# Kernel optimization log

Measured on AMD Instinct MI355X. Metric: run time of the kernel, lower is better.

Reference implementation:

```python
import jax, jax.numpy as jnp
import numpy as np
from jax.scipy.special import logsumexp

EPS = 0.05        # entropic regularization (blur^p)
N_ITERS = 20      # Sinkhorn iterations
N, M, D = 8192, 8192, 64


def setup_inputs() -> dict:
    key = jax.random.key(0)
    k1, k2, k3, k4 = jax.random.split(key, 4)
    return {
        "a": jax.random.uniform(k1, (N,), dtype=jnp.float32),
        "x": jax.random.normal(k2, (N, D), dtype=jnp.float32),
        "b": jax.random.uniform(k3, (M,), dtype=jnp.float32),
        "y": jax.random.normal(k4, (M, D), dtype=jnp.float32),
    }


def reference(a, x, b, y):
    eps = EPS
    # _normalize_weights: probability simplex
    a = a / jnp.sum(a)
    b = b / jnp.sum(b)
    loga = jnp.log(a)
    logb = jnp.log(b)
    # squared-Euclidean cost C_ij = ||x_i - y_j||^2, built via one GEMM (online kernel's math)
    x2 = jnp.sum(x * x, axis=1)            # [N]
    y2 = jnp.sum(y * y, axis=1)            # [M]
    C = x2[:, None] + y2[None, :] - 2.0 * (x @ y.T)   # [N, M]

    # log-domain Sinkhorn: f_i = -eps * LSE_j( log b_j + (g_j - C_ij)/eps )
    def softmin_rows(g_, C_, logw):   # reduce over columns j -> [N]
        return -eps * logsumexp(logw[None, :] + (g_[None, :] - C_) / eps, axis=1)

    def softmin_cols(f_, C_, logw):   # reduce over rows i -> [M]
        return -eps * logsumexp(logw[:, None] + (f_[:, None] - C_) / eps, axis=0)

    def body(i, fg):
        f_, g_ = fg
        f_ = softmin_rows(g_, C, logb)
        g_ = softmin_cols(f_, C, loga)
        return (f_, g_)

    f0 = jnp.zeros_like(a)
    g0 = jnp.zeros_like(b)
    f, g = jax.lax.fori_loop(0, N_ITERS, body, (f0, g0))

    # GeomLoss-style: one final symmetric update from detached potentials (Danskin)
    f_d = jax.lax.stop_gradient(f)
    g_d = jax.lax.stop_gradient(g)
    f_fin = softmin_rows(g_d, C, logb)
    g_fin = softmin_cols(f_d, C, loga)
    # OT_eps(a, b) = <a, f> + <b, g>
    return jnp.sum(a * f_fin) + jnp.sum(b * g_fin)
```

## Files before the change

### kernel.cpp

```cpp
#include <hip/hip_runtime.h>
#include <hip/hip_bf16.h>

#define EPS       0.05f
#define N_ITERS   20
#define NR        8192
#define DIM       64
#define LOG2E     1.4426950408889634f
#define LN2       0.6931471805599453f
#define S2        (2.0f * LOG2E / EPS)
#define EPSLN2    (EPS * LN2)
#define NEGINF    (-1e30f)
#define NSPLIT    16

typedef __attribute__((ext_vector_type(8))) short short8;
typedef __attribute__((ext_vector_type(4))) float float4v;

#define GLD_LDS16(src, dst)                                              \
    __builtin_amdgcn_global_load_lds(                                    \
        (const __attribute__((address_space(1))) void*)(src),            \
        (__attribute__((address_space(3))) void*)(dst), 16, 0, 0)

__device__ __forceinline__ float wave_reduce_sum(float v) {
    #pragma unroll
    for (int m = 1; m < 64; m <<= 1) v += __shfl_xor(v, m, 64);
    return v;
}

__device__ __forceinline__ float merge16_l(const float2* __restrict__ P, int i) {
    float2 p[NSPLIT];
    float M = NEGINF;
    #pragma unroll
    for (int k = 0; k < NSPLIT; k++) {
        p[k] = P[k * NR + i];
        M = fmaxf(M, p[k].x);
    }
    float S = 0.f;
    #pragma unroll
    for (int k = 0; k < NSPLIT; k++)
        S += p[k].y * __builtin_amdgcn_exp2f(p[k].x - M);
    return M + __builtin_amdgcn_logf(S);
}

__global__ void sums_kernel(const float* __restrict__ a, const float* __restrict__ b,
                            float* __restrict__ sums) {
    __shared__ float red[32];
    int tid = threadIdx.x;
    float pa = 0.f, pb = 0.f;
    for (int i = tid; i < NR; i += blockDim.x) { pa += a[i]; pb += b[i]; }
    pa = wave_reduce_sum(pa);
    pb = wave_reduce_sum(pb);
    int wid = tid >> 6, ln = tid & 63;
    if (ln == 0) { red[wid] = pa; red[wid + 16] = pb; }
    __syncthreads();
    if (tid == 0) {
        float sa = 0.f, sb = 0.f;
        int nw = blockDim.x >> 6;
        for (int w = 0; w < nw; w++) { sa += red[w]; sb += red[w + 16]; }
        sums[0] = logf(sa); sums[1] = logf(sb); sums[2] = sa; sums[3] = sb;
    }
}

__global__ void prep_kernel(const float* __restrict__ x, const float* __restrict__ y,
                            const float* __restrict__ a, const float* __restrict__ b,
                            const float* __restrict__ sums,
                            short8* __restrict__ xs, short8* __restrict__ ys,
                            float* __restrict__ x2, float* __restrict__ y2,
                            float* __restrict__ la2, float* __restrict__ lb2,
                            float2* __restrict__ Pb) {
    int gid = blockIdx.x * 256 + threadIdx.x;
    bool isx = gid < NR * 8;
    int cid = isx ? gid : gid - NR * 8;
    int row = cid >> 3;
    int c   = cid & 7;
    const float4* src = (const float4*)(isx ? x : y);
    float4 v0 = src[row * 16 + c * 2];
    float4 v1 = src[row * 16 + c * 2 + 1];

    short8 st;
    st[0] = __bfloat16_as_short(__float2bfloat16(v0.x));
    st[1] = __bfloat16_as_short(__float2bfloat16(v0.y));
    st[2] = __bfloat16_as_short(__float2bfloat16(v0.z));
    st[3] = __bfloat16_as_short(__float2bfloat16(v0.w));
    st[4] = __bfloat16_as_short(__float2bfloat16(v1.x));
    st[5] = __bfloat16_as_short(__float2bfloat16(v1.y));
    st[6] = __bfloat16_as_short(__float2bfloat16(v1.z));
    st[7] = __bfloat16_as_short(__float2bfloat16(v1.w));

    int T = row >> 4, ln = row & 15, f = c >> 2, q = c & 3;
    (isx ? xs : ys)[T * 128 + f * 64 + q * 16 + ln] = st;

    float sq = v0.x*v0.x + v0.y*v0.y + v0.z*v0.z + v0.w*v0.w
             + v1.x*v1.x + v1.y*v1.y + v1.z*v1.z + v1.w*v1.w;
    #pragma unroll
    for (int m = 1; m < 8; m <<= 1) sq += __shfl_xor(sq, m, 64);

    if (c == 0) {
        if (isx) {
            x2[row] = sq;
            la2[row] = (logf(a[row]) - sums[0]) * LOG2E;
        } else {
            y2[row] = sq;
            lb2[row] = (logf(b[row]) - sums[1]) * LOG2E;
            Pb[row] = make_float2(sq * (LOG2E / EPS), 1.0f);
            #pragma unroll
            for (int k = 1; k < NSPLIT; k++)
                Pb[k * NR + row] = make_float2(NEGINF, 0.0f);
        }
    }
}

#define LSE4(acc, c4, mm, ss)                                            \
    {                                                                    \
        float z0 = fmaf(S2, (acc)[0], (c4).x);                           \
        float z1 = fmaf(S2, (acc)[1], (c4).y);                           \
        float z2 = fmaf(S2, (acc)[2], (c4).z);                           \
        float z3 = fmaf(S2, (acc)[3], (c4).w);                           \
        float zm = fmaxf(fmaxf(z0, z1), fmaxf(z2, z3));                  \
        float mn = fmaxf((mm), zm);                                      \
        float e  = __builtin_amdgcn_exp2f((mm) - mn);                    \
        float p  = (__builtin_amdgcn_exp2f(z0 - mn)                      \
                  + __builtin_amdgcn_exp2f(z1 - mn))                     \
                 + (__builtin_amdgcn_exp2f(z2 - mn)                      \
                  + __builtin_amdgcn_exp2f(z3 - mn));                    \
        (ss) = fmaf((ss), e, p);                                         \
        (mm) = mn;                                                       \
    }

__global__ __launch_bounds__(1024, 4) void pass_kernel(
        const short8* __restrict__ matXs,
        const short8* __restrict__ matYs,
        const float2* __restrict__ Pin,
        const float* __restrict__ lw2col,
        float2* __restrict__ Pout) {
    __shared__ __attribute__((aligned(16))) char xlds[65536];
    __shared__ __attribute__((aligned(16))) char ybuf[2][16384];
    __shared__ __attribute__((aligned(16))) float cbl[512];
    __shared__ float2 comb[512][5];

    const int tid = threadIdx.x;
    const int bi  = blockIdx.x;
    const int q   = bi & 15;
    const int rg  = bi >> 4;
    const int rb  = rg * 512;
    const int cb0 = q * 512;

    const int w    = tid >> 6;
    const int lane = tid & 63;
    const int quad = lane >> 4;
    const int ln   = lane & 15;
    const int cst  = w & 3;
    const int rq   = w >> 2;

    const char* xsrc = (const char*)matXs + (size_t)rb * 128;
    #pragma unroll
    for (int r = 0; r < 4; r++)
        GLD_LDS16(xsrc + r * 16384 + tid * 16, &xlds[r * 16384 + w * 1024]);
    const char* ysrc = (const char*)matYs + (size_t)cb0 * 128;
    GLD_LDS16(ysrc + 0 * 16384 + tid * 16, &ybuf[0][w * 1024]);
    GLD_LDS16(ysrc + 1 * 16384 + tid * 16, &ybuf[1][w * 1024]);
    __builtin_amdgcn_sched_barrier(0);

    if (tid < 512) {
        int j = cb0 + tid;
        cbl[tid] = lw2col[j] - merge16_l(Pin, j);
    }
    __builtin_amdgcn_sched_barrier(0);
    __builtin_amdgcn_s_waitcnt(0x0071);
    __builtin_amdgcn_s_barrier();
    __builtin_amdgcn_sched_barrier(0);

    short8 xf0[8], xf1[8];
    {
        const char* xw = &xlds[(rq * 8) * 2048];
        #pragma unroll
        for (int t = 0; t < 8; t++) {
            xf0[t] = *(const short8*)(xw + t * 2048 + lane * 16);
            xf1[t] = *(const short8*)(xw + t * 2048 + 1024 + lane * 16);
        }
    }

    float lm[8], ls[8];
    #pragma unroll
    for (int t = 0; t < 8; t++) { lm[t] = NEGINF; ls[t] = 0.f; }

    #pragma unroll
    for (int c = 0; c < 4; c++) {
        const char* base = &ybuf[c & 1][0];
        #pragma unroll
        for (int uu = 0; uu < 2; uu++) {
            const int u = cst * 2 + uu;
            short8 ya0 = *(const short8*)(base + u * 2048 + lane * 16);
            short8 ya1 = *(const short8*)(base + u * 2048 + 1024 + lane * 16);
            float4 c4  = *(const float4*)(cbl + (c * 8 + u) * 16 + quad * 4);

            #pragma unroll
            for (int tt = 0; tt < 8; tt++) {
                float4v acc = {0.f, 0.f, 0.f, 0.f};
                acc = __builtin_amdgcn_mfma_f32_16x16x32_bf16(ya0, xf0[tt], acc, 0, 0, 0);
                acc = __builtin_amdgcn_mfma_f32_16x16x32_bf16(ya1, xf1[tt], acc, 0, 0, 0);
                LSE4(acc, c4, lm[tt], ls[tt]);
            }
        }
        if (c < 3) {
            __builtin_amdgcn_sched_barrier(0);
            __builtin_amdgcn_s_barrier();
            __builtin_amdgcn_sched_barrier(0);
            if (c < 2)
                GLD_LDS16(ysrc + (c + 2) * 16384 + tid * 16, &ybuf[c & 1][w * 1024]);
            __builtin_amdgcn_sched_barrier(0);
            if (c < 2) __builtin_amdgcn_s_waitcnt(0x0071);
            else       __builtin_amdgcn_s_waitcnt(0x0070);
            __builtin_amdgcn_s_barrier();
            __builtin_amdgcn_sched_barrier(0);
        }
    }

    #pragma unroll
    for (int mask = 16; mask < 64; mask <<= 1) {
        #pragma unroll
        for (int t = 0; t < 8; t++) {
            float mo = __shfl_xor(lm[t], mask, 64);
            float so = __shfl_xor(ls[t], mask, 64);
            float M  = fmaxf(lm[t], mo);
            ls[t] = ls[t] * __builtin_amdgcn_exp2f(lm[t] - M)
                  + so    * __builtin_amdgcn_exp2f(mo    - M);
            lm[t] = M;
        }
    }

    __syncthreads();
    if (lane < 16) {
        #pragma unroll
        for (int t = 0; t < 8; t++)
            comb[rq * 128 + t * 16 + ln][cst] = make_float2(lm[t], ls[t]);
    }
    __syncthreads();

    if (tid < 512) {
        float2 cc0 = comb[tid][0];
        float M = cc0.x, S = cc0.y;
        #pragma unroll
        for (int cc = 1; cc < 4; cc++) {
            float2 p = comb[tid][cc];
            float Mn = fmaxf(M, p.x);
            S = S * __builtin_amdgcn_exp2f(M - Mn)
              + p.y * __builtin_amdgcn_exp2f(p.x - Mn);
            M = Mn;
        }
        Pout[q * NR + rb + tid] = make_float2(M, S);
    }
}

__global__ void reduce1_kernel(const float* __restrict__ a, const float* __restrict__ b,
                               const float* __restrict__ x2, const float* __restrict__ y2,
                               const float2* __restrict__ Pff, const float2* __restrict__ Pgf,
                               float2* __restrict__ red2) {
    __shared__ float red[4];
    int tid = threadIdx.x;
    int r   = blockIdx.x * 128 + (tid & 127);
    bool gs = tid >= 128;
    float L  = merge16_l(gs ? Pgf : Pff, r);
    float sq = gs ? y2[r] : x2[r];
    float wv = gs ? b[r]  : a[r];
    float v  = wv * (sq - EPSLN2 * L);
    v = wave_reduce_sum(v);
    if ((tid & 63) == 0) red[tid >> 6] = v;
    __syncthreads();
    if (tid == 0) red2[blockIdx.x] = make_float2(red[0] + red[1], red[2] + red[3]);
}

__global__ void reduce2_kernel(const float* __restrict__ sums,
                               const float2* __restrict__ red2,
                               float* __restrict__ out) {
    int tid = threadIdx.x;
    float2 v = red2[tid];
    float da = wave_reduce_sum(v.x);
    float db = wave_reduce_sum(v.y);
    if (tid == 0) out[0] = da / sums[2] + db / sums[3];
}

extern "C" void kernel_launch(void* const* d_in, const int* in_sizes, int n_in,
                              void* d_out, int out_size, void* d_ws, size_t ws_size,
                              hipStream_t stream) {
    const float* a = (const float*)d_in[0];
    const float* x = (const float*)d_in[1];
    const float* b = (const float*)d_in[2];
    const float* y = (const float*)d_in[3];

    char* ws = (char*)d_ws;
    short8* xs = (short8*)ws;
    short8* ys = (short8*)(ws + (1 << 20));
    float* fp  = (float*)(ws + (2 << 20));
    float* x2  = fp;
    float* y2  = fp + NR;
    float* la2 = fp + 2 * NR;
    float* lb2 = fp + 3 * NR;
    float2* P   = (float2*)(fp + 4 * NR);
    float2* Pf  = P;
    float2* Pb  = P + NSPLIT * NR;
    float2* Pff = P + 2 * NSPLIT * NR;
    float2* Pgf = P + 3 * NSPLIT * NR;
    float2* red2 = P + 4 * NSPLIT * NR;
    float* sums  = (float*)(red2 + 64);

    sums_kernel<<<1, 1024, 0, stream>>>(a, b, sums);
    prep_kernel<<<(2 * NR * 8) / 256, 256, 0, stream>>>(x, y, a, b, sums,
                                                        xs, ys,
                                                        x2, y2, la2, lb2, Pb);

    for (int it = 0; it < N_ITERS; it++) {
        pass_kernel<<<256, 1024, 0, stream>>>(xs, ys, Pb, lb2, Pf);
        pass_kernel<<<256, 1024, 0, stream>>>(ys, xs, Pf, la2, Pb);
    }
    pass_kernel<<<256, 1024, 0, stream>>>(xs, ys, Pb, lb2, Pff);
    pass_kernel<<<256, 1024, 0, stream>>>(ys, xs, Pf, la2, Pgf);

    reduce1_kernel<<<64, 256, 0, stream>>>(a, b, x2, y2, Pff, Pgf, red2);
    reduce2_kernel<<<1, 64, 0, stream>>>(sums, red2, (float*)d_out);
}
```

Before: 858.1 us.

## Fold cost scale into bf16 x and bias into MFMA accumulator; quad-buffer Y tiles

The S2 scale is folded into the bf16 x operand during prep, and the per-column bias is passed as the initial MFMA accumulator. This removes the per-element FMA in the logsumexp inner loop. The Y tile staging changes from a double buffer to four LDS buffers loaded up front, which drops the mid-loop reload and one barrier per chunk. The cost is 32KB more LDS per block, which may lower occupancy, and bf16 rounding now applies to the scaled x values.

```diff
diff --git a/kernel.cpp b/kernel.cpp
--- a/kernel.cpp
+++ b/kernel.cpp
@@ -76,15 +76,16 @@
     float4 v0 = src[row * 16 + c * 2];
     float4 v1 = src[row * 16 + c * 2 + 1];
 
+    const float sc = isx ? S2 : 1.0f;
     short8 st;
-    st[0] = __bfloat16_as_short(__float2bfloat16(v0.x));
-    st[1] = __bfloat16_as_short(__float2bfloat16(v0.y));
-    st[2] = __bfloat16_as_short(__float2bfloat16(v0.z));
-    st[3] = __bfloat16_as_short(__float2bfloat16(v0.w));
-    st[4] = __bfloat16_as_short(__float2bfloat16(v1.x));
-    st[5] = __bfloat16_as_short(__float2bfloat16(v1.y));
-    st[6] = __bfloat16_as_short(__float2bfloat16(v1.z));
-    st[7] = __bfloat16_as_short(__float2bfloat16(v1.w));
+    st[0] = __bfloat16_as_short(__float2bfloat16(v0.x * sc));
+    st[1] = __bfloat16_as_short(__float2bfloat16(v0.y * sc));
+    st[2] = __bfloat16_as_short(__float2bfloat16(v0.z * sc));
+    st[3] = __bfloat16_as_short(__float2bfloat16(v0.w * sc));
+    st[4] = __bfloat16_as_short(__float2bfloat16(v1.x * sc));
+    st[5] = __bfloat16_as_short(__float2bfloat16(v1.y * sc));
+    st[6] = __bfloat16_as_short(__float2bfloat16(v1.z * sc));
+    st[7] = __bfloat16_as_short(__float2bfloat16(v1.w * sc));
 
     int T = row >> 4, ln = row & 15, f = c >> 2, q = c & 3;
     (isx ? xs : ys)[T * 128 + f * 64 + q * 16 + ln] = st;
@@ -109,14 +110,11 @@
     }
 }
 
-#define LSE4(acc, c4, mm, ss)                                            \
+#define LSE4(acc, mm, ss)                                                \
     {                                                                    \
-        float z0 = fmaf(S2, (acc)[0], (c4).x);                           \
-        float z1 = fmaf(S2, (acc)[1], (c4).y);                           \
-        float z2 = fmaf(S2, (acc)[2], (c4).z);                           \
-        float z3 = fmaf(S2, (acc)[3], (c4).w);                           \
-        float zm = fmaxf(fmaxf(z0, z1), fmaxf(z2, z3));                  \
-        float mn = fmaxf((mm), zm);                                      \
+        float z0 = (acc)[0], z1 = (acc)[1];                              \
+        float z2 = (acc)[2], z3 = (acc)[3];                              \
+        float mn = fmaxf(fmaxf(fmaxf(z0, z1), fmaxf(z2, z3)), (mm));     \
         float e  = __builtin_amdgcn_exp2f((mm) - mn);                    \
         float p  = (__builtin_amdgcn_exp2f(z0 - mn)                      \
                   + __builtin_amdgcn_exp2f(z1 - mn))                     \
@@ -133,7 +131,7 @@
         const float* __restrict__ lw2col,
         float2* __restrict__ Pout) {
     __shared__ __attribute__((aligned(16))) char xlds[65536];
-    __shared__ __attribute__((aligned(16))) char ybuf[2][16384];
+    __shared__ __attribute__((aligned(16))) char ybuf[4][16384];
     __shared__ __attribute__((aligned(16))) float cbl[512];
     __shared__ float2 comb[512][5];
 
@@ -156,8 +154,9 @@
     for (int r = 0; r < 4; r++)
         GLD_LDS16(xsrc + r * 16384 + tid * 16, &xlds[r * 16384 + w * 1024]);
     const char* ysrc = (const char*)matYs + (size_t)cb0 * 128;
-    GLD_LDS16(ysrc + 0 * 16384 + tid * 16, &ybuf[0][w * 1024]);
-    GLD_LDS16(ysrc + 1 * 16384 + tid * 16, &ybuf[1][w * 1024]);
+    #pragma unroll
+    for (int c = 0; c < 4; c++)
+        GLD_LDS16(ysrc + c * 16384 + tid * 16, &ybuf[c][w * 1024]);
     __builtin_amdgcn_sched_barrier(0);
 
     if (tid < 512) {
@@ -165,7 +164,7 @@
         cbl[tid] = lw2col[j] - merge16_l(Pin, j);
     }
     __builtin_amdgcn_sched_barrier(0);
-    __builtin_amdgcn_s_waitcnt(0x0071);
+    __builtin_amdgcn_s_waitcnt(0x0073);
     __builtin_amdgcn_s_barrier();
     __builtin_amdgcn_sched_barrier(0);
 
@@ -185,31 +184,26 @@
 
     #pragma unroll
     for (int c = 0; c < 4; c++) {
-        const char* base = &ybuf[c & 1][0];
+        const char* base = &ybuf[c][0];
         #pragma unroll
         for (int uu = 0; uu < 2; uu++) {
             const int u = cst * 2 + uu;
             short8 ya0 = *(const short8*)(base + u * 2048 + lane * 16);
             short8 ya1 = *(const short8*)(base + u * 2048 + 1024 + lane * 16);
-            float4 c4  = *(const float4*)(cbl + (c * 8 + u) * 16 + quad * 4);
+            float4v cin = *(const float4v*)(cbl + (c * 8 + u) * 16 + quad * 4);
 
             #pragma unroll
             for (int tt = 0; tt < 8; tt++) {
-                float4v acc = {0.f, 0.f, 0.f, 0.f};
-                acc = __builtin_amdgcn_mfma_f32_16x16x32_bf16(ya0, xf0[tt], acc, 0, 0, 0);
+                float4v acc = __builtin_amdgcn_mfma_f32_16x16x32_bf16(ya0, xf0[tt], cin, 0, 0, 0);
                 acc = __builtin_amdgcn_mfma_f32_16x16x32_bf16(ya1, xf1[tt], acc, 0, 0, 0);
-                LSE4(acc, c4, lm[tt], ls[tt]);
+                LSE4(acc, lm[tt], ls[tt]);
             }
         }
         if (c < 3) {
             __builtin_amdgcn_sched_barrier(0);
-            __builtin_amdgcn_s_barrier();
-            __builtin_amdgcn_sched_barrier(0);
-            if (c < 2)
-                GLD_LDS16(ysrc + (c + 2) * 16384 + tid * 16, &ybuf[c & 1][w * 1024]);
-            __builtin_amdgcn_sched_barrier(0);
-            if (c < 2) __builtin_amdgcn_s_waitcnt(0x0071);
-            else       __builtin_amdgcn_s_waitcnt(0x0070);
+            if (c == 0)      __builtin_amdgcn_s_waitcnt(0x0072);
+            else if (c == 1) __builtin_amdgcn_s_waitcnt(0x0071);
+            else             __builtin_amdgcn_s_waitcnt(0x0070);
             __builtin_amdgcn_s_barrier();
             __builtin_amdgcn_sched_barrier(0);
         }
```

Result: no change. 864.7 us (+0.8%).
